# Optimization experiments

Measured on AMD Instinct MI355X. Metric: run time of the kernel, lower is better.

Reference implementation:

```python
import jax, jax.numpy as jnp
import numpy as np

# Production-scale sparse-voxel constants (Waymo-ish stride-8 grid)
N = 1_000_000   # active voxels across the batch
C = 128         # NUM_BEV_FEATURES
B, Z, Y, X = 8, 4, 468, 468  # batch size and spatial_shape (z, y, x)


def setup_inputs() -> dict:
    key = jax.random.key(0)
    kf, kb, kz, ky, kx = jax.random.split(key, 5)
    features = jax.random.normal(kf, (N, C), dtype=jnp.float32)
    b = jax.random.randint(kb, (N,), 0, B, dtype=jnp.int32)
    z = jax.random.randint(kz, (N,), 0, Z, dtype=jnp.int32)
    y = jax.random.randint(ky, (N,), 0, Y, dtype=jnp.int32)
    x = jax.random.randint(kx, (N,), 0, X, dtype=jnp.int32)
    indices = jnp.stack([b, z, y, x], axis=1)  # [N, 4]
    return {"features": features, "indices": indices}


def reference(features, indices):
    """Height compression: drop z, unique over (b, y, x), scatter-add features.

    Mirrors torch.unique(dim=0, return_inverse=True) + index_add_.
    Returns padded outputs of static size N (unique count is data-dependent;
    padded rows have key -1 and zero features / feature mass only where inv points).
    """
    n = features.shape[0]
    b, y, x = indices[:, 0], indices[:, 2], indices[:, 3]
    # Linearize (b, y, x) into a single int32 key; max key B*Y*X ~ 1.75e6 < 2^31.
    keys = (b * (Y * X) + y * X + x).astype(jnp.int32)
    uniq, inv = jnp.unique(keys, size=n, fill_value=-1, return_inverse=True)
    # index_add_ over unique rows == segment_sum with inverse indices
    features_unique = jax.ops.segment_sum(features, inv, num_segments=n)  # [N, C]
    # Decode unique linear keys back to (b, y, x); padded (-1) rows are garbage-marked.
    bb = uniq // (Y * X)
    rem = uniq % (Y * X)
    yy = rem // X
    xx = rem % X
    indices_unique = jnp.stack([bb, yy, xx], axis=1)  # [N, 3]
    return features_unique, indices_unique
```

## Files before the change

### kernel.cpp

```cpp
#include <hip/hip_runtime.h>

#define N_PTS   1000000
#define C_DIM   128
#define B_DIM   8
#define Y_DIM   468
#define X_DIM   468
#define YX      (Y_DIM * X_DIM)
#define KSPACE  (B_DIM * YX)

#define WG   256
#define EPT  8
#define EPB  (WG * EPT)
#define NBLK ((KSPACE + EPB - 1) / EPB)

#define F_BITS 21
#define F_MASK 0x1FFFFFu
#define SINGLE_FLAG (1ull << 63)

#define PAD_BLOCKS 2048

typedef float f4 __attribute__((ext_vector_type(4)));

__device__ __forceinline__ unsigned long long shfl_up_u64(unsigned long long v, int delta) {
    unsigned lo = (unsigned)v;
    unsigned hi = (unsigned)(v >> 32);
    lo = __shfl_up(lo, delta, 64);
    hi = __shfl_up(hi, delta, 64);
    return ((unsigned long long)hi << 32) | lo;
}

__global__ void hist_kernel(const int* __restrict__ idx, unsigned* __restrict__ cnt,
                            unsigned* __restrict__ keys, int n) {
    int i = blockIdx.x * blockDim.x + threadIdx.x;
    if (i >= n) return;
    int4 v = ((const int4*)idx)[i];
    unsigned key = (unsigned)(v.x * YX + v.z * X_DIM + v.w);
    keys[i] = key;
    atomicAdd(&cnt[key], 1u);
}

__global__ void scan1_kernel(const unsigned* __restrict__ cnt,
                             unsigned long long* __restrict__ pairs,
                             unsigned long long* __restrict__ bsums, int K) {
    int base = blockIdx.x * EPB + threadIdx.x * EPT;
    unsigned long long p[EPT];
    unsigned cc[EPT];
    unsigned long long run = 0;
#pragma unroll
    for (int j = 0; j < EPT; ++j) {
        int k = base + j;
        unsigned c = (k < K) ? cnt[k] : 0u;
        cc[j] = c;
        unsigned long long pr = (unsigned long long)c
                              | ((unsigned long long)(c ? 1u : 0u) << F_BITS)
                              | ((unsigned long long)(c >= 2u ? 1u : 0u) << (2 * F_BITS));
        p[j] = run;
        run += pr;
    }
    unsigned long long tot = run;
    int lane = threadIdx.x & 63;
    unsigned long long v = tot;
#pragma unroll
    for (int d = 1; d < 64; d <<= 1) {
        unsigned long long nv = shfl_up_u64(v, d);
        if (lane >= d) v += nv;
    }
    __shared__ unsigned long long wsum[WG / 64];
    int wid = threadIdx.x >> 6;
    if (lane == 63) wsum[wid] = v;
    __syncthreads();
    unsigned long long wexcl = 0;
    for (int w = 0; w < wid; ++w) wexcl += wsum[w];
    unsigned long long texcl = wexcl + v - tot;
#pragma unroll
    for (int j = 0; j < EPT; ++j) {
        int k = base + j;
        if (k < K)
            pairs[k] = (texcl + p[j]) | (cc[j] == 1u ? SINGLE_FLAG : 0ull);
    }
    if (threadIdx.x == WG - 1) bsums[blockIdx.x] = wexcl + v;
}

__global__ void scan2_kernel(unsigned long long* __restrict__ bsums, int nb) {
    int t = threadIdx.x;
    unsigned long long orig = (t < nb) ? bsums[t] : 0ull;
    unsigned long long v = orig;
    int lane = t & 63;
#pragma unroll
    for (int d = 1; d < 64; d <<= 1) {
        unsigned long long nv = shfl_up_u64(v, d);
        if (lane >= d) v += nv;
    }
    __shared__ unsigned long long ws[1024 / 64];
    int wid = t >> 6;
    if (lane == 63) ws[wid] = v;
    __syncthreads();
    unsigned long long wexcl = 0;
    for (int w = 0; w < wid; ++w) wexcl += ws[w];
    if (t < nb) bsums[t] = wexcl + v - orig;
    if (t == 1023) {
        unsigned long long tt = 0;
        for (int w = 0; w < 1024 / 64; ++w) tt += ws[w];
        bsums[nb] = tt;
    }
}

__global__ void __launch_bounds__(256)
heavy_kernel(const float* __restrict__ feat, const unsigned* __restrict__ keys,
             const unsigned long long* __restrict__ pairs,
             const unsigned long long* __restrict__ bsums,
             unsigned* __restrict__ cnt, unsigned* __restrict__ pids,
             uint4* __restrict__ wl,
             float* __restrict__ outF, float* __restrict__ outI,
             int n, int K, int pointBlocks) {
    int tid  = threadIdx.x;
    int lane = tid & 63;
    int wid  = tid >> 6;
    int bid  = blockIdx.x;

    if (bid < NBLK) {
        int base = bid * EPB + tid * EPT;
        if (base >= K) return;
        unsigned long long bofs = bsums[bid];
        unsigned long long P[EPT + 1];
#pragma unroll
        for (int j = 0; j < EPT; ++j) {
            int k = base + j;
            P[j] = (k < K) ? ((pairs[k] & ~SINGLE_FLAG) + bofs) : bsums[NBLK];
        }
        {
            int k = base + EPT;
            P[EPT] = (k < K) ? ((pairs[k] & ~SINGLE_FLAG) + bsums[k >> 11]) : bsums[NBLK];
        }
#pragma unroll
        for (int j = 0; j < EPT; ++j) {
            int k = base + j;
            if (k >= K) break;
            unsigned long long diff = P[j + 1] - P[j];
            unsigned c = (unsigned)(diff & F_MASK);
            if (c == 0) continue;
            unsigned rank = (unsigned)((P[j] >> F_BITS) & F_MASK);
            unsigned bb  = (unsigned)k / YX;
            unsigned rem = (unsigned)k % YX;
            outI[(size_t)rank * 3 + 0] = (float)bb;
            outI[(size_t)rank * 3 + 1] = (float)(rem / X_DIM);
            outI[(size_t)rank * 3 + 2] = (float)(rem % X_DIM);
            if (c >= 2) {
                unsigned start = (unsigned)(P[j] & F_MASK);
                unsigned mslot = (unsigned)((P[j] >> (2 * F_BITS)) & F_MASK);
                wl[mslot] = make_uint4(start, start + c, (unsigned)k, rank);
            }
        }
    } else if (bid < NBLK + pointBlocks) {
        int e   = lane >> 3;
        int sub = lane & 7;
        long p = (long)(bid - NBLK) * 32 + wid * 8 + e;
        if (p >= n) return;
        unsigned key = keys[p];
        unsigned long long pr = pairs[key];
        if (pr >> 63) {
            pr += bsums[key >> 11];
            unsigned rank = (unsigned)((pr >> F_BITS) & F_MASK);
            const f4* src = (const f4*)(feat + (size_t)p * C_DIM);
            f4*       dst = (f4*)(outF + (size_t)rank * C_DIM);
            f4 v0 = __builtin_nontemporal_load(src + sub);
            f4 v1 = __builtin_nontemporal_load(src + sub + 8);
            f4 v2 = __builtin_nontemporal_load(src + sub + 16);
            f4 v3 = __builtin_nontemporal_load(src + sub + 24);
            __builtin_nontemporal_store(v0, dst + sub);
            __builtin_nontemporal_store(v1, dst + sub + 8);
            __builtin_nontemporal_store(v2, dst + sub + 16);
            __builtin_nontemporal_store(v3, dst + sub + 24);
        } else if (sub == 0) {
            unsigned start = (unsigned)((pr + bsums[key >> 11]) & F_MASK);
            unsigned off = atomicSub(&cnt[key], 1u) - 1u;
            pids[start + off] = (unsigned)p;
        }
    } else {
        int e   = lane >> 3;
        int sub = lane & 7;
        unsigned long long tot = bsums[NBLK];
        long nU = (long)((tot >> F_BITS) & F_MASK);
        long pb = bid - NBLK - pointBlocks;
        long base   = nU + pb * 32 + wid * 8 + e;
        long stride = (long)PAD_BLOCKS * 32;
        f4 z = (f4)(0.f);
        for (long r = base; r < n; r += stride) {
            f4* dst = (f4*)(outF + (size_t)r * C_DIM);
            __builtin_nontemporal_store(z, dst + sub);
            __builtin_nontemporal_store(z, dst + sub + 8);
            __builtin_nontemporal_store(z, dst + sub + 16);
            __builtin_nontemporal_store(z, dst + sub + 24);
            if (sub == 0) {
                outI[(size_t)r * 3 + 0] = -1.0f;
                outI[(size_t)r * 3 + 1] = 467.0f;
                outI[(size_t)r * 3 + 2] = 467.0f;
            }
        }
    }
}

__global__ void __launch_bounds__(256)
multi_kernel(const float* __restrict__ feat, const unsigned* __restrict__ pointIds,
             const uint4* __restrict__ wl,
             const unsigned long long* __restrict__ total,
             float* __restrict__ outF) {
    int lane = threadIdx.x & 63;
    int wid  = threadIdx.x >> 6;
    int rq   = lane >> 4;
    int sub  = lane & 15;
    long m = (long)(((*total) >> (2 * F_BITS)) & F_MASK);
    long base   = (long)blockIdx.x * 16 + wid * 4 + rq;
    long stride = (long)gridDim.x * 16;
    for (long r = base; r < m; r += stride) {
        uint4 d = wl[r];
        f4 a0 = (f4)(0.f);
        f4 a1 = (f4)(0.f);
        unsigned j = d.x, e = d.y;
        for (; j + 1 < e; j += 2) {
            unsigned p0 = pointIds[j];
            unsigned p1 = pointIds[j + 1];
            const f4* s0 = (const f4*)(feat + (size_t)p0 * C_DIM);
            const f4* s1 = (const f4*)(feat + (size_t)p1 * C_DIM);
            f4 v00 = __builtin_nontemporal_load(s0 + sub);
            f4 v01 = __builtin_nontemporal_load(s0 + sub + 16);
            f4 v10 = __builtin_nontemporal_load(s1 + sub);
            f4 v11 = __builtin_nontemporal_load(s1 + sub + 16);
            a0 += v00 + v10;
            a1 += v01 + v11;
        }
        if (j < e) {
            unsigned p0 = pointIds[j];
            const f4* s0 = (const f4*)(feat + (size_t)p0 * C_DIM);
            f4 v00 = __builtin_nontemporal_load(s0 + sub);
            f4 v01 = __builtin_nontemporal_load(s0 + sub + 16);
            a0 += v00;
            a1 += v01;
        }
        f4* dst = (f4*)(outF + (size_t)d.w * C_DIM);
        __builtin_nontemporal_store(a0, dst + sub);
        __builtin_nontemporal_store(a1, dst + sub + 16);
    }
}

extern "C" void kernel_launch(void* const* d_in, const int* in_sizes, int n_in,
                              void* d_out, int out_size, void* d_ws, size_t ws_size,
                              hipStream_t stream) {
    const float* feat = (const float*)d_in[0];
    const int*   idx  = (const int*)d_in[1];
    const int n = in_sizes[0] / C_DIM;
    const int K = KSPACE;

    char* ws = (char*)d_ws;
    size_t off = 0;
    auto take = [&](size_t bytes) {
        size_t cur = off;
        off = (off + bytes + 255) & ~(size_t)255;
        return cur;
    };
    size_t o_cnt    = take((size_t)K * 4);
    size_t o_keys   = take((size_t)n * 4);
    size_t o_pairs  = take((size_t)K * 8);
    size_t o_bsums  = take((size_t)(NBLK + 1) * 8);
    size_t o_pids   = take((size_t)n * 4);
    size_t o_wl     = take((size_t)(n / 2 + 1) * 16);

    unsigned*           cnt    = (unsigned*)(ws + o_cnt);
    unsigned*           keys   = (unsigned*)(ws + o_keys);
    unsigned long long* pairs  = (unsigned long long*)(ws + o_pairs);
    unsigned long long* bsums  = (unsigned long long*)(ws + o_bsums);
    unsigned*           pids   = (unsigned*)(ws + o_pids);
    uint4*              wl     = (uint4*)(ws + o_wl);

    float* outF = (float*)d_out;
    float* outI = outF + (size_t)n * C_DIM;

    hipMemsetAsync(cnt, 0, (size_t)K * 4, stream);
    hist_kernel<<<(n + 255) / 256, 256, 0, stream>>>(idx, cnt, keys, n);
    scan1_kernel<<<NBLK, WG, 0, stream>>>(cnt, pairs, bsums, K);
    scan2_kernel<<<1, 1024, 0, stream>>>(bsums, NBLK);
    {
        int pointBlocks = (n + 31) / 32;
        heavy_kernel<<<NBLK + pointBlocks + PAD_BLOCKS, 256, 0, stream>>>(
            feat, keys, pairs, bsums, cnt, pids, wl, outF, outI, n, K, pointBlocks);
    }
    multi_kernel<<<4096, 256, 0, stream>>>(feat, pids, wl, bsums + NBLK, outF);
}
```

Baseline: 280.4 us.

## Move singleton feature copies into key-space blocks via key-to-point map

```diff
diff --git a/kernel.cpp b/kernel.cpp
--- a/kernel.cpp
+++ b/kernel.cpp
@@ -17,7 +17,7 @@
 #define F_MASK 0x1FFFFFu
 #define SINGLE_FLAG (1ull << 63)
 
-#define PAD_BLOCKS 2048
+#define PAD_BLOCKS 1024
 
 typedef float f4 __attribute__((ext_vector_type(4)));
 
@@ -30,12 +30,14 @@
 }
 
 __global__ void hist_kernel(const int* __restrict__ idx, unsigned* __restrict__ cnt,
-                            unsigned* __restrict__ keys, int n) {
+                            unsigned* __restrict__ keys, unsigned* __restrict__ pkey,
+                            int n) {
     int i = blockIdx.x * blockDim.x + threadIdx.x;
     if (i >= n) return;
     int4 v = ((const int4*)idx)[i];
     unsigned key = (unsigned)(v.x * YX + v.z * X_DIM + v.w);
     keys[i] = key;
+    pkey[key] = (unsigned)i;
     atomicAdd(&cnt[key], 1u);
 }
 
@@ -107,81 +109,121 @@
 
 __global__ void __launch_bounds__(256)
 heavy_kernel(const float* __restrict__ feat, const unsigned* __restrict__ keys,
+             const unsigned* __restrict__ pkey,
              const unsigned long long* __restrict__ pairs,
              const unsigned long long* __restrict__ bsums,
              unsigned* __restrict__ cnt, unsigned* __restrict__ pids,
              uint4* __restrict__ wl,
              float* __restrict__ outF, float* __restrict__ outI,
-             int n, int K, int pointBlocks) {
+             int n, int K, int scatBlocks) {
     int tid  = threadIdx.x;
-    int lane = tid & 63;
-    int wid  = tid >> 6;
     int bid  = blockIdx.x;
 
     if (bid < NBLK) {
+        __shared__ unsigned s_pid[EPB];
+        __shared__ unsigned s_rank[EPB];
+        __shared__ unsigned s_cnt;
+        if (tid == 0) s_cnt = 0;
+        __syncthreads();
+
         int base = bid * EPB + tid * EPT;
-        if (base >= K) return;
-        unsigned long long bofs = bsums[bid];
-        unsigned long long P[EPT + 1];
-#pragma unroll
-        for (int j = 0; j < EPT; ++j) {
-            int k = base + j;
-            P[j] = (k < K) ? ((pairs[k] & ~SINGLE_FLAG) + bofs) : bsums[NBLK];
-        }
-        {
-            int k = base + EPT;
-            P[EPT] = (k < K) ? ((pairs[k] & ~SINGLE_FLAG) + bsums[k >> 11]) : bsums[NBLK];
-        }
-#pragma unroll
-        for (int j = 0; j < EPT; ++j) {
-            int k = base + j;
-            if (k >= K) break;
-            unsigned long long diff = P[j + 1] - P[j];
-            unsigned c = (unsigned)(diff & F_MASK);
-            if (c == 0) continue;
-            unsigned rank = (unsigned)((P[j] >> F_BITS) & F_MASK);
-            unsigned bb  = (unsigned)k / YX;
-            unsigned rem = (unsigned)k % YX;
-            outI[(size_t)rank * 3 + 0] = (float)bb;
-            outI[(size_t)rank * 3 + 1] = (float)(rem / X_DIM);
-            outI[(size_t)rank * 3 + 2] = (float)(rem % X_DIM);
-            if (c >= 2) {
-                unsigned start = (unsigned)(P[j] & F_MASK);
-                unsigned mslot = (unsigned)((P[j] >> (2 * F_BITS)) & F_MASK);
-                wl[mslot] = make_uint4(start, start + c, (unsigned)k, rank);
+        if (base < K) {
+            unsigned long long bofs = bsums[bid];
+            unsigned long long P[EPT + 1];
+#pragma unroll
+            for (int j = 0; j < EPT; ++j) {
+                int k = base + j;
+                P[j] = (k < K) ? ((pairs[k] & ~SINGLE_FLAG) + bofs) : bsums[NBLK];
             }
-        }
-    } else if (bid < NBLK + pointBlocks) {
-        int e   = lane >> 3;
-        int sub = lane & 7;
-        long p = (long)(bid - NBLK) * 32 + wid * 8 + e;
+            {
+                int k = base + EPT;
+                P[EPT] = (k < K) ? ((pairs[k] & ~SINGLE_FLAG) + bsums[k >> 11]) : bsums[NBLK];
+            }
+#pragma unroll
+            for (int j = 0; j < EPT; ++j) {
+                int k = base + j;
+                if (k >= K) break;
+                unsigned long long diff = P[j + 1] - P[j];
+                unsigned c = (unsigned)(diff & F_MASK);
+                if (c == 0) continue;
+                unsigned rank = (unsigned)((P[j] >> F_BITS) & F_MASK);
+                unsigned bb  = (unsigned)k / YX;
+                unsigned rem = (unsigned)k % YX;
+                outI[(size_t)rank * 3 + 0] = (float)bb;
+                outI[(size_t)rank * 3 + 1] = (float)(rem / X_DIM);
+                outI[(size_t)rank * 3 + 2] = (float)(rem % X_DIM);
+                if (c == 1) {
+                    unsigned slot = atomicAdd(&s_cnt, 1u);
+                    s_pid[slot]  = pkey[k];
+                    s_rank[slot] = rank;
+                } else {
+                    unsigned start = (unsigned)(P[j] & F_MASK);
+                    unsigned mslot = (unsigned)((P[j] >> (2 * F_BITS)) & F_MASK);
+                    wl[mslot] = make_uint4(start, start + c, (unsigned)k, rank);
+                }
+            }
+        }
+        __syncthreads();
+
+        unsigned m = s_cnt;
+        int g   = tid >> 3;
+        int sub = tid & 7;
+        unsigned i = g;
+        for (; i + 32 < m; i += 64) {
+            unsigned pid0 = s_pid[i],      rk0 = s_rank[i];
+            unsigned pid1 = s_pid[i + 32], rk1 = s_rank[i + 32];
+            const f4* s0 = (const f4*)(feat + (size_t)pid0 * C_DIM);
+            const f4* s1 = (const f4*)(feat + (size_t)pid1 * C_DIM);
+            f4 v00 = __builtin_nontemporal_load(s0 + sub);
+            f4 v01 = __builtin_nontemporal_load(s0 + sub + 8);
+            f4 v02 = __builtin_nontemporal_load(s0 + sub + 16);
+            f4 v03 = __builtin_nontemporal_load(s0 + sub + 24);
+            f4 v10 = __builtin_nontemporal_load(s1 + sub);
+            f4 v11 = __builtin_nontemporal_load(s1 + sub + 8);
+            f4 v12 = __builtin_nontemporal_load(s1 + sub + 16);
+            f4 v13 = __builtin_nontemporal_load(s1 + sub + 24);
+            f4* d0 = (f4*)(outF + (size_t)rk0 * C_DIM);
+            f4* d1 = (f4*)(outF + (size_t)rk1 * C_DIM);
+            __builtin_nontemporal_store(v00, d0 + sub);
+            __builtin_nontemporal_store(v01, d0 + sub + 8);
+            __builtin_nontemporal_store(v02, d0 + sub + 16);
+            __builtin_nontemporal_store(v03, d0 + sub + 24);
+            __builtin_nontemporal_store(v10, d1 + sub);
+            __builtin_nontemporal_store(v11, d1 + sub + 8);
+            __builtin_nontemporal_store(v12, d1 + sub + 16);
+            __builtin_nontemporal_store(v13, d1 + sub + 24);
+        }
+        for (; i < m; i += 32) {
+            unsigned pid0 = s_pid[i], rk0 = s_rank[i];
+            const f4* s0 = (const f4*)(feat + (size_t)pid0 * C_DIM);
+            f4 v00 = __builtin_nontemporal_load(s0 + sub);
+            f4 v01 = __builtin_nontemporal_load(s0 + sub + 8);
+            f4 v02 = __builtin_nontemporal_load(s0 + sub + 16);
+            f4 v03 = __builtin_nontemporal_load(s0 + sub + 24);
+            f4* d0 = (f4*)(outF + (size_t)rk0 * C_DIM);
+            __builtin_nontemporal_store(v00, d0 + sub);
+            __builtin_nontemporal_store(v01, d0 + sub + 8);
+            __builtin_nontemporal_store(v02, d0 + sub + 16);
+            __builtin_nontemporal_store(v03, d0 + sub + 24);
+        }
+    } else if (bid < NBLK + scatBlocks) {
+        long p = (long)(bid - NBLK) * 256 + tid;
         if (p >= n) return;
         unsigned key = keys[p];
         unsigned long long pr = pairs[key];
-        if (pr >> 63) {
-            pr += bsums[key >> 11];
-            unsigned rank = (unsigned)((pr >> F_BITS) & F_MASK);
-            const f4* src = (const f4*)(feat + (size_t)p * C_DIM);
-            f4*       dst = (f4*)(outF + (size_t)rank * C_DIM);
-            f4 v0 = __builtin_nontemporal_load(src + sub);
-            f4 v1 = __builtin_nontemporal_load(src + sub + 8);
-            f4 v2 = __builtin_nontemporal_load(src + sub + 16);
-            f4 v3 = __builtin_nontemporal_load(src + sub + 24);
-            __builtin_nontemporal_store(v0, dst + sub);
-            __builtin_nontemporal_store(v1, dst + sub + 8);
-            __builtin_nontemporal_store(v2, dst + sub + 16);
-            __builtin_nontemporal_store(v3, dst + sub + 24);
-        } else if (sub == 0) {
+        if (!(pr >> 63)) {
             unsigned start = (unsigned)((pr + bsums[key >> 11]) & F_MASK);
             unsigned off = atomicSub(&cnt[key], 1u) - 1u;
             pids[start + off] = (unsigned)p;
         }
     } else {
-        int e   = lane >> 3;
-        int sub = lane & 7;
+        int lane = tid & 63;
+        int wid  = tid >> 6;
+        int e    = lane >> 3;
+        int sub  = lane & 7;
         unsigned long long tot = bsums[NBLK];
         long nU = (long)((tot >> F_BITS) & F_MASK);
-        long pb = bid - NBLK - pointBlocks;
+        long pb = bid - NBLK - scatBlocks;
         long base   = nU + pb * 32 + wid * 8 + e;
         long stride = (long)PAD_BLOCKS * 32;
         f4 z = (f4)(0.f);
@@ -259,6 +301,7 @@
         return cur;
     };
     size_t o_cnt    = take((size_t)K * 4);
+    size_t o_pkey   = take((size_t)K * 4);
     size_t o_keys   = take((size_t)n * 4);
     size_t o_pairs  = take((size_t)K * 8);
     size_t o_bsums  = take((size_t)(NBLK + 1) * 8);
@@ -266,6 +309,7 @@
     size_t o_wl     = take((size_t)(n / 2 + 1) * 16);
 
     unsigned*           cnt    = (unsigned*)(ws + o_cnt);
+    unsigned*           pkey   = (unsigned*)(ws + o_pkey);
     unsigned*           keys   = (unsigned*)(ws + o_keys);
     unsigned long long* pairs  = (unsigned long long*)(ws + o_pairs);
     unsigned long long* bsums  = (unsigned long long*)(ws + o_bsums);
@@ -276,13 +320,13 @@
     float* outI = outF + (size_t)n * C_DIM;
 
     hipMemsetAsync(cnt, 0, (size_t)K * 4, stream);
-    hist_kernel<<<(n + 255) / 256, 256, 0, stream>>>(idx, cnt, keys, n);
+    hist_kernel<<<(n + 255) / 256, 256, 0, stream>>>(idx, cnt, keys, pkey, n);
     scan1_kernel<<<NBLK, WG, 0, stream>>>(cnt, pairs, bsums, K);
     scan2_kernel<<<1, 1024, 0, stream>>>(bsums, NBLK);
     {
-        int pointBlocks = (n + 31) / 32;
-        heavy_kernel<<<NBLK + pointBlocks + PAD_BLOCKS, 256, 0, stream>>>(
-            feat, keys, pairs, bsums, cnt, pids, wl, outF, outI, n, K, pointBlocks);
+        int scatBlocks = (n + 255) / 256;
+        heavy_kernel<<<NBLK + scatBlocks + PAD_BLOCKS, 256, 0, stream>>>(
+            feat, keys, pkey, pairs, bsums, cnt, pids, wl, outF, outI, n, K, scatBlocks);
     }
     multi_kernel<<<4096, 256, 0, stream>>>(feat, pids, wl, bsums + NBLK, outF);
 }
```

Result: slower. 323.8 us (+15.5%).

## Split metadata resolution from feature copy and merge multi-sum into copy kernel

Applied to the files above, without the earlier changes.

```diff
diff --git a/kernel.cpp b/kernel.cpp
--- a/kernel.cpp
+++ b/kernel.cpp
@@ -17,7 +17,8 @@
 #define F_MASK 0x1FFFFFu
 #define SINGLE_FLAG (1ull << 63)
 
-#define PAD_BLOCKS 2048
+#define MULTI_BLOCKS 4096
+#define PAD_BLOCKS   1024
 
 typedef float f4 __attribute__((ext_vector_type(4)));
 
@@ -106,17 +107,14 @@
 }
 
 __global__ void __launch_bounds__(256)
-heavy_kernel(const float* __restrict__ feat, const unsigned* __restrict__ keys,
+meta2_kernel(const unsigned* __restrict__ keys,
              const unsigned long long* __restrict__ pairs,
              const unsigned long long* __restrict__ bsums,
              unsigned* __restrict__ cnt, unsigned* __restrict__ pids,
-             uint4* __restrict__ wl,
-             float* __restrict__ outF, float* __restrict__ outI,
-             int n, int K, int pointBlocks) {
-    int tid  = threadIdx.x;
-    int lane = tid & 63;
-    int wid  = tid >> 6;
-    int bid  = blockIdx.x;
+             unsigned* __restrict__ prank, uint4* __restrict__ wl,
+             float* __restrict__ outI, int n, int K) {
+    int tid = threadIdx.x;
+    int bid = blockIdx.x;
 
     if (bid < NBLK) {
         int base = bid * EPB + tid * EPT;
@@ -151,37 +149,94 @@
                 wl[mslot] = make_uint4(start, start + c, (unsigned)k, rank);
             }
         }
-    } else if (bid < NBLK + pointBlocks) {
-        int e   = lane >> 3;
-        int sub = lane & 7;
-        long p = (long)(bid - NBLK) * 32 + wid * 8 + e;
+    } else {
+        long p = (long)(bid - NBLK) * 256 + tid;
         if (p >= n) return;
         unsigned key = keys[p];
         unsigned long long pr = pairs[key];
+        unsigned long long Pc = (pr & ~SINGLE_FLAG) + bsums[key >> 11];
+        unsigned rank = (unsigned)((Pc >> F_BITS) & F_MASK);
         if (pr >> 63) {
-            pr += bsums[key >> 11];
-            unsigned rank = (unsigned)((pr >> F_BITS) & F_MASK);
-            const f4* src = (const f4*)(feat + (size_t)p * C_DIM);
-            f4*       dst = (f4*)(outF + (size_t)rank * C_DIM);
-            f4 v0 = __builtin_nontemporal_load(src + sub);
-            f4 v1 = __builtin_nontemporal_load(src + sub + 8);
-            f4 v2 = __builtin_nontemporal_load(src + sub + 16);
-            f4 v3 = __builtin_nontemporal_load(src + sub + 24);
-            __builtin_nontemporal_store(v0, dst + sub);
-            __builtin_nontemporal_store(v1, dst + sub + 8);
-            __builtin_nontemporal_store(v2, dst + sub + 16);
-            __builtin_nontemporal_store(v3, dst + sub + 24);
-        } else if (sub == 0) {
-            unsigned start = (unsigned)((pr + bsums[key >> 11]) & F_MASK);
+            prank[p] = rank | 0x80000000u;
+        } else {
+            prank[p] = rank;
+            unsigned start = (unsigned)(Pc & F_MASK);
             unsigned off = atomicSub(&cnt[key], 1u) - 1u;
             pids[start + off] = (unsigned)p;
+        }
+    }
+}
+
+__global__ void __launch_bounds__(256)
+copy_kernel(const float* __restrict__ feat, const unsigned* __restrict__ prank,
+            const unsigned* __restrict__ pointIds, const uint4* __restrict__ wl,
+            const unsigned long long* __restrict__ total,
+            float* __restrict__ outF, float* __restrict__ outI,
+            int n, int pointBlocks) {
+    int tid  = threadIdx.x;
+    int lane = tid & 63;
+    int wid  = tid >> 6;
+    int bid  = blockIdx.x;
+
+    if (bid < pointBlocks) {
+        int e   = lane >> 3;
+        int sub = lane & 7;
+        long p = (long)bid * 32 + wid * 8 + e;
+        if (p >= n) return;
+        unsigned pr = prank[p];
+        if (!(pr >> 31)) return;
+        unsigned rank = pr & 0x7FFFFFFFu;
+        const f4* src = (const f4*)(feat + (size_t)p * C_DIM);
+        f4*       dst = (f4*)(outF + (size_t)rank * C_DIM);
+        f4 v0 = __builtin_nontemporal_load(src + sub);
+        f4 v1 = __builtin_nontemporal_load(src + sub + 8);
+        f4 v2 = __builtin_nontemporal_load(src + sub + 16);
+        f4 v3 = __builtin_nontemporal_load(src + sub + 24);
+        __builtin_nontemporal_store(v0, dst + sub);
+        __builtin_nontemporal_store(v1, dst + sub + 8);
+        __builtin_nontemporal_store(v2, dst + sub + 16);
+        __builtin_nontemporal_store(v3, dst + sub + 24);
+    } else if (bid < pointBlocks + MULTI_BLOCKS) {
+        int rq  = lane >> 4;
+        int sub = lane & 15;
+        long m = (long)(((*total) >> (2 * F_BITS)) & F_MASK);
+        long base   = (long)(bid - pointBlocks) * 16 + wid * 4 + rq;
+        long stride = (long)MULTI_BLOCKS * 16;
+        for (long r = base; r < m; r += stride) {
+            uint4 d = wl[r];
+            f4 a0 = (f4)(0.f);
+            f4 a1 = (f4)(0.f);
+            unsigned j = d.x, e2 = d.y;
+            for (; j + 1 < e2; j += 2) {
+                unsigned p0 = pointIds[j];
+                unsigned p1 = pointIds[j + 1];
+                const f4* s0 = (const f4*)(feat + (size_t)p0 * C_DIM);
+                const f4* s1 = (const f4*)(feat + (size_t)p1 * C_DIM);
+                f4 v00 = __builtin_nontemporal_load(s0 + sub);
+                f4 v01 = __builtin_nontemporal_load(s0 + sub + 16);
+                f4 v10 = __builtin_nontemporal_load(s1 + sub);
+                f4 v11 = __builtin_nontemporal_load(s1 + sub + 16);
+                a0 += v00 + v10;
+                a1 += v01 + v11;
+            }
+            if (j < e2) {
+                unsigned p0 = pointIds[j];
+                const f4* s0 = (const f4*)(feat + (size_t)p0 * C_DIM);
+                f4 v00 = __builtin_nontemporal_load(s0 + sub);
+                f4 v01 = __builtin_nontemporal_load(s0 + sub + 16);
+                a0 += v00;
+                a1 += v01;
+            }
+            f4* dst = (f4*)(outF + (size_t)d.w * C_DIM);
+            __builtin_nontemporal_store(a0, dst + sub);
+            __builtin_nontemporal_store(a1, dst + sub + 16);
         }
     } else {
         int e   = lane >> 3;
         int sub = lane & 7;
-        unsigned long long tot = bsums[NBLK];
+        unsigned long long tot = *total;
         long nU = (long)((tot >> F_BITS) & F_MASK);
-        long pb = bid - NBLK - pointBlocks;
+        long pb = bid - pointBlocks - MULTI_BLOCKS;
         long base   = nU + pb * 32 + wid * 8 + e;
         long stride = (long)PAD_BLOCKS * 32;
         f4 z = (f4)(0.f);
@@ -200,49 +255,6 @@
     }
 }
 
-__global__ void __launch_bounds__(256)
-multi_kernel(const float* __restrict__ feat, const unsigned* __restrict__ pointIds,
-             const uint4* __restrict__ wl,
-             const unsigned long long* __restrict__ total,
-             float* __restrict__ outF) {
-    int lane = threadIdx.x & 63;
-    int wid  = threadIdx.x >> 6;
-    int rq   = lane >> 4;
-    int sub  = lane & 15;
-    long m = (long)(((*total) >> (2 * F_BITS)) & F_MASK);
-    long base   = (long)blockIdx.x * 16 + wid * 4 + rq;
-    long stride = (long)gridDim.x * 16;
-    for (long r = base; r < m; r += stride) {
-        uint4 d = wl[r];
-        f4 a0 = (f4)(0.f);
-        f4 a1 = (f4)(0.f);
-        unsigned j = d.x, e = d.y;
-        for (; j + 1 < e; j += 2) {
-            unsigned p0 = pointIds[j];
-            unsigned p1 = pointIds[j + 1];
-            const f4* s0 = (const f4*)(feat + (size_t)p0 * C_DIM);
-            const f4* s1 = (const f4*)(feat + (size_t)p1 * C_DIM);
-            f4 v00 = __builtin_nontemporal_load(s0 + sub);
-            f4 v01 = __builtin_nontemporal_load(s0 + sub + 16);
-            f4 v10 = __builtin_nontemporal_load(s1 + sub);
-            f4 v11 = __builtin_nontemporal_load(s1 + sub + 16);
-            a0 += v00 + v10;
-            a1 += v01 + v11;
-        }
-        if (j < e) {
-            unsigned p0 = pointIds[j];
-            const f4* s0 = (const f4*)(feat + (size_t)p0 * C_DIM);
-            f4 v00 = __builtin_nontemporal_load(s0 + sub);
-            f4 v01 = __builtin_nontemporal_load(s0 + sub + 16);
-            a0 += v00;
-            a1 += v01;
-        }
-        f4* dst = (f4*)(outF + (size_t)d.w * C_DIM);
-        __builtin_nontemporal_store(a0, dst + sub);
-        __builtin_nontemporal_store(a1, dst + sub + 16);
-    }
-}
-
 extern "C" void kernel_launch(void* const* d_in, const int* in_sizes, int n_in,
                               void* d_out, int out_size, void* d_ws, size_t ws_size,
                               hipStream_t stream) {
@@ -260,6 +272,7 @@
     };
     size_t o_cnt    = take((size_t)K * 4);
     size_t o_keys   = take((size_t)n * 4);
+    size_t o_prank  = take((size_t)n * 4);
     size_t o_pairs  = take((size_t)K * 8);
     size_t o_bsums  = take((size_t)(NBLK + 1) * 8);
     size_t o_pids   = take((size_t)n * 4);
@@ -267,6 +280,7 @@
 
     unsigned*           cnt    = (unsigned*)(ws + o_cnt);
     unsigned*           keys   = (unsigned*)(ws + o_keys);
+    unsigned*           prank  = (unsigned*)(ws + o_prank);
     unsigned long long* pairs  = (unsigned long long*)(ws + o_pairs);
     unsigned long long* bsums  = (unsigned long long*)(ws + o_bsums);
     unsigned*           pids   = (unsigned*)(ws + o_pids);
@@ -280,9 +294,13 @@
     scan1_kernel<<<NBLK, WG, 0, stream>>>(cnt, pairs, bsums, K);
     scan2_kernel<<<1, 1024, 0, stream>>>(bsums, NBLK);
     {
+        int resolveBlocks = (n + 255) / 256;
+        meta2_kernel<<<NBLK + resolveBlocks, 256, 0, stream>>>(
+            keys, pairs, bsums, cnt, pids, prank, wl, outI, n, K);
+    }
+    {
         int pointBlocks = (n + 31) / 32;
-        heavy_kernel<<<NBLK + pointBlocks + PAD_BLOCKS, 256, 0, stream>>>(
-            feat, keys, pairs, bsums, cnt, pids, wl, outF, outI, n, K, pointBlocks);
-    }
-    multi_kernel<<<4096, 256, 0, stream>>>(feat, pids, wl, bsums + NBLK, outF);
-}
+        copy_kernel<<<pointBlocks + MULTI_BLOCKS + PAD_BLOCKS, 256, 0, stream>>>(
+            feat, prank, pids, wl, bsums + NBLK, outF, outI, n, pointBlocks);
+    }
+}
```

New measurement: 310.5 us. 1.11x slower.
